# Performance work log

Hardware: AMD Instinct MI355X
Metric: run time of the kernel (lower is better)

Reference implementation:

```python
import jax, jax.numpy as jnp
import numpy as np

D_MODEL = 1024
HEADS = 16
D_K = D_MODEL // HEADS
NEG_INF = -1e10


def setup_inputs() -> dict:
    key = jax.random.key(0)
    ks = jax.random.split(key, 10)
    n, s = 2, 2048
    inp = {
        "value": jax.random.normal(ks[0], (n, s, D_MODEL), dtype=jnp.float32),
        "key": jax.random.normal(ks[1], (n, s, D_MODEL), dtype=jnp.float32),
        "query": jax.random.normal(ks[2], (n, s, D_MODEL), dtype=jnp.float32),
        "mask": jax.random.randint(ks[3], (n, 1, s, s), 0, 2, dtype=jnp.int32),
        # torch.nn.Linear weights are [out, in]; y = x @ W.T (+ b)
        "Wq": jax.random.normal(ks[4], (D_MODEL, D_MODEL), dtype=jnp.float32) * (D_MODEL ** -0.5),
        "Wk": jax.random.normal(ks[5], (D_MODEL, D_MODEL), dtype=jnp.float32) * (D_MODEL ** -0.5),
        "Wv": jax.random.normal(ks[6], (D_MODEL, D_MODEL), dtype=jnp.float32) * (D_MODEL ** -0.5),
        "Wo": jax.random.normal(ks[7], (D_MODEL, D_MODEL), dtype=jnp.float32) * (D_MODEL ** -0.5),
        "bo": jax.random.normal(ks[8], (D_MODEL,), dtype=jnp.float32) * 0.01,
    }
    return inp


def reference(value, key, query, mask, Wq, Wk, Wv, Wo, bo):
    n, q_len, _ = query.shape
    # projections (Linear, no bias): x @ W.T
    q = (query @ Wq.T).reshape(n, q_len, HEADS, D_K)
    k = (key @ Wk.T).reshape(n, key.shape[1], HEADS, D_K)
    v = (value @ Wv.T).reshape(n, value.shape[1], HEADS, D_K)
    scores = jnp.einsum('nqhd,nkhd->nhqk', q, k)  # [n,h,q,k]
    scores = jnp.where(mask == 0, jnp.float32(NEG_INF), scores)
    attn = jax.nn.softmax(scores / jnp.sqrt(jnp.float32(D_K)), axis=-1)
    out = jnp.einsum('nhql,nlhd->nqhd', attn, v).reshape(n, q_len, D_MODEL)
    return out @ Wo.T + bo
```

## Files before the change

kernel.cpp:

```cpp
#include <hip/hip_runtime.h>
#include <hip/hip_bf16.h>
#include <stdint.h>

#define SEQ     2048
#define NBATCH  2
#define DMODEL  1024
#define NH      16
#define DKH     64

typedef __bf16 bf16;
typedef __attribute__((ext_vector_type(8))) __bf16 bf16x8;
typedef __attribute__((ext_vector_type(4))) __bf16 bf16x4;
typedef __attribute__((ext_vector_type(4))) float  f32x4;

static __device__ __forceinline__ f32x4 mfma16(bf16x8 a, bf16x8 b, f32x4 c) {
    return __builtin_amdgcn_mfma_f32_16x16x32_bf16(a, b, c, 0, 0, 0);
}

typedef const __attribute__((address_space(1))) void* gas_cptr;
typedef __attribute__((address_space(3))) void*       las_ptr;
#define GLDS16(g, l) __builtin_amdgcn_global_load_lds((gas_cptr)(g), (las_ptr)(l), 16, 0, 0)

__global__ __launch_bounds__(256) void cvt_all_k(const float* __restrict__ q,
                                                 const float* __restrict__ k,
                                                 const float* __restrict__ v,
                                                 const float* __restrict__ wq,
                                                 const float* __restrict__ wk,
                                                 const float* __restrict__ wv,
                                                 const float* __restrict__ wo,
                                                 bf16* __restrict__ qb, bf16* __restrict__ kb,
                                                 bf16* __restrict__ vb, bf16* __restrict__ wqb,
                                                 bf16* __restrict__ wkb, bf16* __restrict__ wvb,
                                                 bf16* __restrict__ wob) {
    const float* src; bf16* dst; int n4;
    const int NX4 = (NBATCH * SEQ * DMODEL) / 4, NW4 = (DMODEL * DMODEL) / 4;
    switch (blockIdx.y) {
        case 0: src = q;  dst = qb;  n4 = NX4; break;
        case 1: src = k;  dst = kb;  n4 = NX4; break;
        case 2: src = v;  dst = vb;  n4 = NX4; break;
        case 3: src = wq; dst = wqb; n4 = NW4; break;
        case 4: src = wk; dst = wkb; n4 = NW4; break;
        case 5: src = wv; dst = wvb; n4 = NW4; break;
        default: src = wo; dst = wob; n4 = NW4; break;
    }
    int stride = gridDim.x * blockDim.x;
    for (int i = blockIdx.x * blockDim.x + threadIdx.x; i < n4; i += stride) {
        f32x4 f = ((const f32x4*)src)[i];
        bf16x4 o;
#pragma unroll
        for (int j = 0; j < 4; j++) o[j] = (bf16)f[j];
        ((bf16x4*)dst)[i] = o;
    }
}

__global__ __launch_bounds__(256) void pack_mask_k(const int* __restrict__ mask,
                                                   unsigned long long* __restrict__ bits,
                                                   int nwords) {
    int wave  = (blockIdx.x * blockDim.x + threadIdx.x) >> 6;
    int lane  = threadIdx.x & 63;
    int nwtot = (gridDim.x * blockDim.x) >> 6;
    for (int w = wave; w < nwords; w += nwtot) {
        int m = mask[(size_t)w * 64 + lane];
        unsigned long long b = __ballot(m != 0);
        if (lane == 0) bits[w] = b;
    }
}

__global__ __launch_bounds__(256) void qkv_gemm(const bf16* __restrict__ Xq,
                                                const bf16* __restrict__ Xk,
                                                const bf16* __restrict__ Xv,
                                                const bf16* __restrict__ Wq,
                                                const bf16* __restrict__ Wk,
                                                const bf16* __restrict__ Wv,
                                                bf16* __restrict__ Qo,
                                                bf16* __restrict__ Ko,
                                                bf16* __restrict__ Vto) {
    __shared__ bf16 As[128 * 32], Bs[128 * 32];
    const int z = blockIdx.z;
    const bf16* A = (z == 0) ? Xq : (z == 1) ? Xk : Xv;
    const bf16* W = (z == 0) ? Wq : (z == 1) ? Wk : Wv;
    const int bm = blockIdx.x * 128, bn = blockIdx.y * 128;
    const int tid = threadIdx.x, wave = tid >> 6, lane = tid & 63;
    const int wm = wave >> 1, wn = wave & 1, lo = lane & 15, hi = lane >> 4;

    const int r0 = wave * 32 + (lane >> 2);
    const int c8 = (lane & 3) * 8;
    const bf16* Ag = A + (size_t)(bm + r0) * DMODEL + c8;
    const bf16* Bg = W + (size_t)(bn + r0) * DMODEL + c8;
    bf16* lA = &As[wave * 1024];
    bf16* lB = &Bs[wave * 1024];

    f32x4 acc[4][4];
#pragma unroll
    for (int i = 0; i < 4; i++)
#pragma unroll
        for (int j = 0; j < 4; j++) acc[i][j] = 0.0f;

    for (int k0 = 0; k0 < DMODEL; k0 += 32) {
        __syncthreads();
        GLDS16(Ag + k0, lA);
        GLDS16(Ag + k0 + (size_t)16 * DMODEL, lA + 512);
        GLDS16(Bg + k0, lB);
        GLDS16(Bg + k0 + (size_t)16 * DMODEL, lB + 512);
        __syncthreads();

        bf16x8 a[4], b[4];
#pragma unroll
        for (int t = 0; t < 4; t++) {
            a[t] = *(const bf16x8*)&As[(wm * 64 + t * 16 + lo) * 32 + hi * 8];
            b[t] = *(const bf16x8*)&Bs[(wn * 64 + t * 16 + lo) * 32 + hi * 8];
        }
#pragma unroll
        for (int tm = 0; tm < 4; tm++)
#pragma unroll
            for (int tn = 0; tn < 4; tn++)
                acc[tm][tn] = mfma16(a[tm], b[tn], acc[tm][tn]);
    }

    if (z < 2) {
        bf16* O = (z == 0) ? Qo : Ko;
#pragma unroll
        for (int tm = 0; tm < 4; tm++)
#pragma unroll
            for (int tn = 0; tn < 4; tn++)
#pragma unroll
                for (int r = 0; r < 4; r++) {
                    int m = bm + wm * 64 + tm * 16 + hi * 4 + r;
                    int o = bn + wn * 64 + tn * 16 + lo;
                    int nidx = m >> 11, sq = m & 2047;
                    int hh = o >> 6, d = o & 63;
                    O[(((size_t)nidx * NH + hh) * SEQ + sq) * DKH + d] = (bf16)acc[tm][tn][r];
                }
    } else {
#pragma unroll
        for (int tm = 0; tm < 4; tm++)
#pragma unroll
            for (int tn = 0; tn < 4; tn++)
#pragma unroll
                for (int r = 0; r < 4; r++) {
                    int m = bm + wm * 64 + tm * 16 + hi * 4 + r;
                    int o = bn + wn * 64 + tn * 16 + lo;
                    int nidx = m >> 11, sq = m & 2047;
                    int hh = o >> 6, d = o & 63;
                    Vto[(((size_t)nidx * NH + hh) * DKH + d) * SEQ + sq] = (bf16)acc[tm][tn][r];
                }
    }
}

__global__ __launch_bounds__(256, 5) void attn_k(const bf16* __restrict__ Q,
                                                 const bf16* __restrict__ K,
                                                 const bf16* __restrict__ Vt,
                                                 const unsigned long long* __restrict__ mbits,
                                                 bf16* __restrict__ Op0,
                                                 bf16* __restrict__ Op1,
                                                 float* __restrict__ Lp) {
    __shared__ bf16 Ks[64 * 72];
    __shared__ bf16 Vs[64 * 72];
    __shared__ bf16 Ps[64 * 72];

    const int bid = blockIdx.x;
    const int xcd = bid & 7, j = bid >> 3;
    const int hd = xcd * 4 + (j & 3);
    const int qb = (j >> 2) & 31;
    const int ks = j >> 7;
    const int n = hd >> 4, h = hd & 15;

    const int tid = threadIdx.x, wave = tid >> 6, lane = tid & 63;
    const int lo = lane & 15, hi = lane >> 4;

    const size_t headoff = (size_t)hd * SEQ * DKH;
    const bf16* Qh = Q + headoff;
    const bf16* Kh = K + headoff;
    const bf16* Vh = Vt + headoff;

    const int qrow = qb * 64 + wave * 16 + lo;
    const bf16x8 aq0 = *(const bf16x8*)(Qh + (size_t)qrow * DKH + hi * 8);
    const bf16x8 aq1 = *(const bf16x8*)(Qh + (size_t)qrow * DKH + 32 + hi * 8);

    bf16x8 ones;
#pragma unroll
    for (int i = 0; i < 8; i++) ones[i] = (bf16)1.0f;

    f32x4 oacc[4];
#pragma unroll
    for (int t = 0; t < 4; t++) oacc[t] = 0.0f;
    f32x4 lacc; lacc = 0.0f;

    const unsigned long long* mb = mbits + ((size_t)n * SEQ + qb * 64 + wave * 16) * (SEQ / 64);
    const float c = 0.18033688f;

    const int kbeg = ks * 1024, kend = kbeg + 1024;

    const int srow = tid >> 3, sseg = tid & 7;
    const bf16* Kg = Kh + (size_t)srow * DKH + sseg * 8;
    const bf16* Vg = Vh + (size_t)srow * SEQ + sseg * 8;

    bf16x8 rk0 = *(const bf16x8*)(Kg + (size_t)kbeg * DKH);
    bf16x8 rk1 = *(const bf16x8*)(Kg + (size_t)(kbeg + 32) * DKH);
    bf16x8 rv0 = *(const bf16x8*)(Vg + kbeg);
    bf16x8 rv1 = *(const bf16x8*)(Vg + (size_t)32 * SEQ + kbeg);

    for (int k0 = kbeg; k0 < kend; k0 += 64) {
        __syncthreads();
        *(bf16x8*)&Ks[srow * 72 + sseg * 8]        = rk0;
        *(bf16x8*)&Ks[(srow + 32) * 72 + sseg * 8] = rk1;
        *(bf16x8*)&Vs[srow * 72 + sseg * 8]        = rv0;
        *(bf16x8*)&Vs[(srow + 32) * 72 + sseg * 8] = rv1;
        if (k0 + 64 < kend) {
            rk0 = *(const bf16x8*)(Kg + (size_t)(k0 + 64) * DKH);
            rk1 = *(const bf16x8*)(Kg + (size_t)(k0 + 96) * DKH);
            rv0 = *(const bf16x8*)(Vg + k0 + 64);
            rv1 = *(const bf16x8*)(Vg + (size_t)32 * SEQ + k0 + 64);
        }
        __syncthreads();

        unsigned long long w64[4];
#pragma unroll
        for (int r = 0; r < 4; r++) w64[r] = mb[(size_t)(hi * 4 + r) * (SEQ / 64) + (k0 >> 6)];

        f32x4 s[4];
#pragma unroll
        for (int tn = 0; tn < 4; tn++) {
            const int kr = (tn * 16 + lo) * 72;
            bf16x8 b0 = *(const bf16x8*)&Ks[kr + hi * 8];
            bf16x8 b1 = *(const bf16x8*)&Ks[kr + 32 + hi * 8];
            f32x4 z4; z4 = 0.0f;
            z4 = mfma16(aq0, b0, z4);
            z4 = mfma16(aq1, b1, z4);
            s[tn] = z4;
        }

#pragma unroll
        for (int r = 0; r < 4; r++) {
            unsigned wlo = (unsigned)(w64[r] >> lo);
            unsigned whi = (unsigned)(w64[r] >> (lo + 32));
#pragma unroll
            for (int tn = 0; tn < 4; tn++) {
                unsigned bit = ((tn < 2 ? wlo : whi) >> ((tn & 1) * 16)) & 1u;
                float pv = exp2f(s[tn][r] * c);
                pv = bit ? pv : 0.0f;
                Ps[(wave * 16 + hi * 4 + r) * 72 + tn * 16 + lo] = (bf16)pv;
            }
        }
        asm volatile("s_waitcnt lgkmcnt(0)" ::: "memory");

        bf16x8 ap0 = *(const bf16x8*)&Ps[(wave * 16 + lo) * 72 + hi * 8];
        bf16x8 ap1 = *(const bf16x8*)&Ps[(wave * 16 + lo) * 72 + 32 + hi * 8];
#pragma unroll
        for (int td = 0; td < 4; td++) {
            bf16x8 b0 = *(const bf16x8*)&Vs[(td * 16 + lo) * 72 + hi * 8];
            bf16x8 b1 = *(const bf16x8*)&Vs[(td * 16 + lo) * 72 + 32 + hi * 8];
            oacc[td] = mfma16(ap0, b0, oacc[td]);
            oacc[td] = mfma16(ap1, b1, oacc[td]);
        }
        lacc = mfma16(ap0, ones, lacc);
        lacc = mfma16(ap1, ones, lacc);
    }

    bf16* Op = ks ? Op1 : Op0;
#pragma unroll
    for (int td = 0; td < 4; td++)
#pragma unroll
        for (int r = 0; r < 4; r++) {
            int q = qb * 64 + wave * 16 + hi * 4 + r;
            int d = td * 16 + lo;
            Op[((size_t)n * SEQ + q) * DMODEL + h * 64 + d] = (bf16)oacc[td][r];
        }
    if (lo == 0) {
#pragma unroll
        for (int r = 0; r < 4; r++) {
            int q = qb * 64 + wave * 16 + hi * 4 + r;
            Lp[(size_t)ks * (NBATCH * NH * SEQ) + ((size_t)(n * NH + h) * SEQ) + q] = lacc[r];
        }
    }
}

__global__ __launch_bounds__(256) void merge_k(const bf16* __restrict__ o0,
                                               const bf16* __restrict__ o1,
                                               const float* __restrict__ lp,
                                               bf16* __restrict__ Aout) {
    int t = blockIdx.x * blockDim.x + threadIdx.x;
    int q = t >> 7;
    int h = (t >> 3) & 15;
    int n = q >> 11;
    bf16x8 a = ((const bf16x8*)o0)[t];
    bf16x8 b = ((const bf16x8*)o1)[t];
    int li = (n * NH + h) * SEQ + (q & 2047);
    float l = lp[li] + lp[NBATCH * NH * SEQ + li];
    float rl = 1.0f / l;
    bf16x8 o;
#pragma unroll
    for (int i = 0; i < 8; i++) o[i] = (bf16)(((float)a[i] + (float)b[i]) * rl);
    ((bf16x8*)Aout)[t] = o;
}

__global__ __launch_bounds__(256) void out_gemm(const bf16* __restrict__ A,
                                                const bf16* __restrict__ W,
                                                const float* __restrict__ bias,
                                                float* __restrict__ Out) {
    __shared__ bf16 As[128 * 32], Bs[128 * 32];
    const int bm = blockIdx.x * 128, bn = blockIdx.y * 128;
    const int tid = threadIdx.x, wave = tid >> 6, lane = tid & 63;
    const int wm = wave >> 1, wn = wave & 1, lo = lane & 15, hi = lane >> 4;

    const int r0 = wave * 32 + (lane >> 2);
    const int c8 = (lane & 3) * 8;
    const bf16* Ag = A + (size_t)(bm + r0) * DMODEL + c8;
    const bf16* Bg = W + (size_t)(bn + r0) * DMODEL + c8;
    bf16* lA = &As[wave * 1024];
    bf16* lB = &Bs[wave * 1024];

    f32x4 acc[4][4];
#pragma unroll
    for (int i = 0; i < 4; i++)
#pragma unroll
        for (int j = 0; j < 4; j++) acc[i][j] = 0.0f;

    for (int k0 = 0; k0 < DMODEL; k0 += 32) {
        __syncthreads();
        GLDS16(Ag + k0, lA);
        GLDS16(Ag + k0 + (size_t)16 * DMODEL, lA + 512);
        GLDS16(Bg + k0, lB);
        GLDS16(Bg + k0 + (size_t)16 * DMODEL, lB + 512);
        __syncthreads();

        bf16x8 a[4], b[4];
#pragma unroll
        for (int t = 0; t < 4; t++) {
            a[t] = *(const bf16x8*)&As[(wm * 64 + t * 16 + lo) * 32 + hi * 8];
            b[t] = *(const bf16x8*)&Bs[(wn * 64 + t * 16 + lo) * 32 + hi * 8];
        }
#pragma unroll
        for (int tm = 0; tm < 4; tm++)
#pragma unroll
            for (int tn = 0; tn < 4; tn++)
                acc[tm][tn] = mfma16(a[tm], b[tn], acc[tm][tn]);
    }

#pragma unroll
    for (int tm = 0; tm < 4; tm++)
#pragma unroll
        for (int tn = 0; tn < 4; tn++) {
            int o = bn + wn * 64 + tn * 16 + lo;
            float bv = bias[o];
#pragma unroll
            for (int r = 0; r < 4; r++) {
                int m = bm + wm * 64 + tm * 16 + hi * 4 + r;
                Out[(size_t)m * DMODEL + o] = acc[tm][tn][r] + bv;
            }
        }
}

extern "C" void kernel_launch(void* const* d_in, const int* in_sizes, int n_in,
                              void* d_out, int out_size, void* d_ws, size_t ws_size,
                              hipStream_t stream) {
    const float* value = (const float*)d_in[0];
    const float* key   = (const float*)d_in[1];
    const float* query = (const float*)d_in[2];
    const int*   mask  = (const int*)d_in[3];
    const float* Wq    = (const float*)d_in[4];
    const float* Wk    = (const float*)d_in[5];
    const float* Wv    = (const float*)d_in[6];
    const float* Wo    = (const float*)d_in[7];
    const float* bo    = (const float*)d_in[8];
    float* out = (float*)d_out;

    char* ws = (char*)d_ws;
    bf16* Qws = (bf16*)(ws);
    bf16* Kws = (bf16*)(ws + (8u  << 20));
    bf16* Vt  = (bf16*)(ws + (16u << 20));
    bf16* Xqb = (bf16*)(ws + (24u << 20));
    bf16* Xkb = (bf16*)(ws + (32u << 20));
    bf16* Xvb = (bf16*)(ws + (40u << 20));
    bf16* Wqb = (bf16*)(ws + (48u << 20));
    bf16* Wkb = (bf16*)(ws + (50u << 20));
    bf16* Wvb = (bf16*)(ws + (52u << 20));
    bf16* Wob = (bf16*)(ws + (54u << 20));
    unsigned long long* mbits = (unsigned long long*)(ws + (56u << 20));
    bf16*  Op0 = Xqb;
    bf16*  Op1 = Xkb;
    bf16*  Aws = Xvb;
    float* Lp  = (float*)Wqb;

    cvt_all_k<<<dim3(1024, 7), 256, 0, stream>>>(query, key, value, Wq, Wk, Wv, Wo,
                                                 Xqb, Xkb, Xvb, Wqb, Wkb, Wvb, Wob);
    pack_mask_k<<<1024, 256, 0, stream>>>(mask, mbits, NBATCH * SEQ * (SEQ / 64));
    qkv_gemm<<<dim3(32, 8, 3), 256, 0, stream>>>(Xqb, Xkb, Xvb, Wqb, Wkb, Wvb, Qws, Kws, Vt);
    attn_k<<<2048, 256, 0, stream>>>(Qws, Kws, Vt, mbits, Op0, Op1, Lp);
    merge_k<<<2048, 256, 0, stream>>>(Op0, Op1, Lp, Aws);
    out_gemm<<<dim3(32, 8), 256, 0, stream>>>(Aws, Wob, bo, out);
}
```

Before: 299.7 us.

## Fuse mask packing, deepen QKV K-step, fold softmax scale, widen attention blocks

Mask bit-packing is folded into the conversion kernel as an extra grid row, which removes one launch. The QKV GEMM now loads 64-wide K slabs per barrier pair instead of 32, halving the number of synchronisations. The softmax scale is folded into Q at projection time, so the exp in attention no longer needs a multiply. The attention kernel uses 512-thread blocks covering 128 query rows, so each K/V tile staged in shared memory is reused by twice as many waves, with one load per thread instead of two. The trade-offs are higher register and LDS pressure per block and slightly different rounding, since the scale is applied before the bf16 cast of Q.

Measured after the change: 360.1 us. 20.1% more time.

```diff
diff --git a/kernel.cpp b/kernel.cpp
--- a/kernel.cpp
+++ b/kernel.cpp
@@ -8,6 +8,8 @@
 #define NH      16
 #define DKH     64
 
+#define CSCALE  0.18033688f
+
 typedef __bf16 bf16;
 typedef __attribute__((ext_vector_type(8))) __bf16 bf16x8;
 typedef __attribute__((ext_vector_type(4))) __bf16 bf16x4;
@@ -21,17 +23,31 @@
 typedef __attribute__((address_space(3))) void*       las_ptr;
 #define GLDS16(g, l) __builtin_amdgcn_global_load_lds((gas_cptr)(g), (las_ptr)(l), 16, 0, 0)
 
-__global__ __launch_bounds__(256) void cvt_all_k(const float* __restrict__ q,
-                                                 const float* __restrict__ k,
-                                                 const float* __restrict__ v,
-                                                 const float* __restrict__ wq,
-                                                 const float* __restrict__ wk,
-                                                 const float* __restrict__ wv,
-                                                 const float* __restrict__ wo,
-                                                 bf16* __restrict__ qb, bf16* __restrict__ kb,
-                                                 bf16* __restrict__ vb, bf16* __restrict__ wqb,
-                                                 bf16* __restrict__ wkb, bf16* __restrict__ wvb,
-                                                 bf16* __restrict__ wob) {
+__global__ __launch_bounds__(256) void cvt_pack_k(const float* __restrict__ q,
+                                                  const float* __restrict__ k,
+                                                  const float* __restrict__ v,
+                                                  const float* __restrict__ wq,
+                                                  const float* __restrict__ wk,
+                                                  const float* __restrict__ wv,
+                                                  const float* __restrict__ wo,
+                                                  const int* __restrict__ mask,
+                                                  bf16* __restrict__ qb, bf16* __restrict__ kb,
+                                                  bf16* __restrict__ vb, bf16* __restrict__ wqb,
+                                                  bf16* __restrict__ wkb, bf16* __restrict__ wvb,
+                                                  bf16* __restrict__ wob,
+                                                  unsigned long long* __restrict__ bits) {
+    if (blockIdx.y == 7) {
+        const int nwords = NBATCH * SEQ * (SEQ / 64);
+        int wave  = (blockIdx.x * blockDim.x + threadIdx.x) >> 6;
+        int lane  = threadIdx.x & 63;
+        int nwtot = (gridDim.x * blockDim.x) >> 6;
+        for (int w = wave; w < nwords; w += nwtot) {
+            int m = mask[(size_t)w * 64 + lane];
+            unsigned long long b = __ballot(m != 0);
+            if (lane == 0) bits[w] = b;
+        }
+        return;
+    }
     const float* src; bf16* dst; int n4;
     const int NX4 = (NBATCH * SEQ * DMODEL) / 4, NW4 = (DMODEL * DMODEL) / 4;
     switch (blockIdx.y) {
@@ -53,19 +69,6 @@
     }
 }
 
-__global__ __launch_bounds__(256) void pack_mask_k(const int* __restrict__ mask,
-                                                   unsigned long long* __restrict__ bits,
-                                                   int nwords) {
-    int wave  = (blockIdx.x * blockDim.x + threadIdx.x) >> 6;
-    int lane  = threadIdx.x & 63;
-    int nwtot = (gridDim.x * blockDim.x) >> 6;
-    for (int w = wave; w < nwords; w += nwtot) {
-        int m = mask[(size_t)w * 64 + lane];
-        unsigned long long b = __ballot(m != 0);
-        if (lane == 0) bits[w] = b;
-    }
-}
-
 __global__ __launch_bounds__(256) void qkv_gemm(const bf16* __restrict__ Xq,
                                                 const bf16* __restrict__ Xk,
                                                 const bf16* __restrict__ Xv,
@@ -75,7 +78,7 @@
                                                 bf16* __restrict__ Qo,
                                                 bf16* __restrict__ Ko,
                                                 bf16* __restrict__ Vto) {
-    __shared__ bf16 As[128 * 32], Bs[128 * 32];
+    __shared__ bf16 As0[128 * 32], As1[128 * 32], Bs0[128 * 32], Bs1[128 * 32];
     const int z = blockIdx.z;
     const bf16* A = (z == 0) ? Xq : (z == 1) ? Xk : Xv;
     const bf16* W = (z == 0) ? Wq : (z == 1) ? Wk : Wv;
@@ -87,8 +90,7 @@
     const int c8 = (lane & 3) * 8;
     const bf16* Ag = A + (size_t)(bm + r0) * DMODEL + c8;
     const bf16* Bg = W + (size_t)(bn + r0) * DMODEL + c8;
-    bf16* lA = &As[wave * 1024];
-    bf16* lB = &Bs[wave * 1024];
+    const int lof = wave * 1024;
 
     f32x4 acc[4][4];
 #pragma unroll
@@ -96,27 +98,42 @@
 #pragma unroll
         for (int j = 0; j < 4; j++) acc[i][j] = 0.0f;
 
-    for (int k0 = 0; k0 < DMODEL; k0 += 32) {
-        __syncthreads();
-        GLDS16(Ag + k0, lA);
-        GLDS16(Ag + k0 + (size_t)16 * DMODEL, lA + 512);
-        GLDS16(Bg + k0, lB);
-        GLDS16(Bg + k0 + (size_t)16 * DMODEL, lB + 512);
+    for (int k0 = 0; k0 < DMODEL; k0 += 64) {
+        __syncthreads();
+        GLDS16(Ag + k0,                          As0 + lof);
+        GLDS16(Ag + k0 + (size_t)16 * DMODEL,    As0 + lof + 512);
+        GLDS16(Ag + k0 + 32,                     As1 + lof);
+        GLDS16(Ag + k0 + 32 + (size_t)16 * DMODEL, As1 + lof + 512);
+        GLDS16(Bg + k0,                          Bs0 + lof);
+        GLDS16(Bg + k0 + (size_t)16 * DMODEL,    Bs0 + lof + 512);
+        GLDS16(Bg + k0 + 32,                     Bs1 + lof);
+        GLDS16(Bg + k0 + 32 + (size_t)16 * DMODEL, Bs1 + lof + 512);
         __syncthreads();
 
         bf16x8 a[4], b[4];
 #pragma unroll
         for (int t = 0; t < 4; t++) {
-            a[t] = *(const bf16x8*)&As[(wm * 64 + t * 16 + lo) * 32 + hi * 8];
-            b[t] = *(const bf16x8*)&Bs[(wn * 64 + t * 16 + lo) * 32 + hi * 8];
+            a[t] = *(const bf16x8*)&As0[(wm * 64 + t * 16 + lo) * 32 + hi * 8];
+            b[t] = *(const bf16x8*)&Bs0[(wn * 64 + t * 16 + lo) * 32 + hi * 8];
         }
 #pragma unroll
         for (int tm = 0; tm < 4; tm++)
 #pragma unroll
             for (int tn = 0; tn < 4; tn++)
                 acc[tm][tn] = mfma16(a[tm], b[tn], acc[tm][tn]);
-    }
-
+#pragma unroll
+        for (int t = 0; t < 4; t++) {
+            a[t] = *(const bf16x8*)&As1[(wm * 64 + t * 16 + lo) * 32 + hi * 8];
+            b[t] = *(const bf16x8*)&Bs1[(wn * 64 + t * 16 + lo) * 32 + hi * 8];
+        }
+#pragma unroll
+        for (int tm = 0; tm < 4; tm++)
+#pragma unroll
+            for (int tn = 0; tn < 4; tn++)
+                acc[tm][tn] = mfma16(a[tm], b[tn], acc[tm][tn]);
+    }
+
+    const float osc = (z == 0) ? CSCALE : 1.0f;
     if (z < 2) {
         bf16* O = (z == 0) ? Qo : Ko;
 #pragma unroll
@@ -129,7 +146,7 @@
                     int o = bn + wn * 64 + tn * 16 + lo;
                     int nidx = m >> 11, sq = m & 2047;
                     int hh = o >> 6, d = o & 63;
-                    O[(((size_t)nidx * NH + hh) * SEQ + sq) * DKH + d] = (bf16)acc[tm][tn][r];
+                    O[(((size_t)nidx * NH + hh) * SEQ + sq) * DKH + d] = (bf16)(acc[tm][tn][r] * osc);
                 }
     } else {
 #pragma unroll
@@ -147,7 +164,7 @@
     }
 }
 
-__global__ __launch_bounds__(256, 5) void attn_k(const bf16* __restrict__ Q,
+__global__ __launch_bounds__(512, 8) void attn_k(const bf16* __restrict__ Q,
                                                  const bf16* __restrict__ K,
                                                  const bf16* __restrict__ Vt,
                                                  const unsigned long long* __restrict__ mbits,
@@ -156,13 +173,13 @@
                                                  float* __restrict__ Lp) {
     __shared__ bf16 Ks[64 * 72];
     __shared__ bf16 Vs[64 * 72];
-    __shared__ bf16 Ps[64 * 72];
+    __shared__ bf16 Ps[128 * 72];
 
     const int bid = blockIdx.x;
     const int xcd = bid & 7, j = bid >> 3;
     const int hd = xcd * 4 + (j & 3);
-    const int qb = (j >> 2) & 31;
-    const int ks = j >> 7;
+    const int qb = (j >> 2) & 15;
+    const int ks = j >> 6;
     const int n = hd >> 4, h = hd & 15;
 
     const int tid = threadIdx.x, wave = tid >> 6, lane = tid & 63;
@@ -173,7 +190,7 @@
     const bf16* Kh = K + headoff;
     const bf16* Vh = Vt + headoff;
 
-    const int qrow = qb * 64 + wave * 16 + lo;
+    const int qrow = qb * 128 + wave * 16 + lo;
     const bf16x8 aq0 = *(const bf16x8*)(Qh + (size_t)qrow * DKH + hi * 8);
     const bf16x8 aq1 = *(const bf16x8*)(Qh + (size_t)qrow * DKH + 32 + hi * 8);
 
@@ -186,31 +203,25 @@
     for (int t = 0; t < 4; t++) oacc[t] = 0.0f;
     f32x4 lacc; lacc = 0.0f;
 
-    const unsigned long long* mb = mbits + ((size_t)n * SEQ + qb * 64 + wave * 16) * (SEQ / 64);
-    const float c = 0.18033688f;
+    const unsigned long long* mb = mbits + ((size_t)n * SEQ + qb * 128 + wave * 16) * (SEQ / 64);
 
     const int kbeg = ks * 1024, kend = kbeg + 1024;
 
     const int srow = tid >> 3, sseg = tid & 7;
     const bf16* Kg = Kh + (size_t)srow * DKH + sseg * 8;
     const bf16* Vg = Vh + (size_t)srow * SEQ + sseg * 8;
-
-    bf16x8 rk0 = *(const bf16x8*)(Kg + (size_t)kbeg * DKH);
-    bf16x8 rk1 = *(const bf16x8*)(Kg + (size_t)(kbeg + 32) * DKH);
-    bf16x8 rv0 = *(const bf16x8*)(Vg + kbeg);
-    bf16x8 rv1 = *(const bf16x8*)(Vg + (size_t)32 * SEQ + kbeg);
+    const int si = srow * 72 + sseg * 8;
+
+    bf16x8 rk = *(const bf16x8*)(Kg + (size_t)kbeg * DKH);
+    bf16x8 rv = *(const bf16x8*)(Vg + kbeg);
 
     for (int k0 = kbeg; k0 < kend; k0 += 64) {
         __syncthreads();
-        *(bf16x8*)&Ks[srow * 72 + sseg * 8]        = rk0;
-        *(bf16x8*)&Ks[(srow + 32) * 72 + sseg * 8] = rk1;
-        *(bf16x8*)&Vs[srow * 72 + sseg * 8]        = rv0;
-        *(bf16x8*)&Vs[(srow + 32) * 72 + sseg * 8] = rv1;
+        *(bf16x8*)&Ks[si] = rk;
+        *(bf16x8*)&Vs[si] = rv;
         if (k0 + 64 < kend) {
-            rk0 = *(const bf16x8*)(Kg + (size_t)(k0 + 64) * DKH);
-            rk1 = *(const bf16x8*)(Kg + (size_t)(k0 + 96) * DKH);
-            rv0 = *(const bf16x8*)(Vg + k0 + 64);
-            rv1 = *(const bf16x8*)(Vg + (size_t)32 * SEQ + k0 + 64);
+            rk = *(const bf16x8*)(Kg + (size_t)(k0 + 64) * DKH);
+            rv = *(const bf16x8*)(Vg + k0 + 64);
         }
         __syncthreads();
 
@@ -237,7 +248,7 @@
 #pragma unroll
             for (int tn = 0; tn < 4; tn++) {
                 unsigned bit = ((tn < 2 ? wlo : whi) >> ((tn & 1) * 16)) & 1u;
-                float pv = exp2f(s[tn][r] * c);
+                float pv = exp2f(s[tn][r]);
                 pv = bit ? pv : 0.0f;
                 Ps[(wave * 16 + hi * 4 + r) * 72 + tn * 16 + lo] = (bf16)pv;
             }
@@ -262,14 +273,14 @@
     for (int td = 0; td < 4; td++)
 #pragma unroll
         for (int r = 0; r < 4; r++) {
-            int q = qb * 64 + wave * 16 + hi * 4 + r;
+            int q = qb * 128 + wave * 16 + hi * 4 + r;
             int d = td * 16 + lo;
             Op[((size_t)n * SEQ + q) * DMODEL + h * 64 + d] = (bf16)oacc[td][r];
         }
     if (lo == 0) {
 #pragma unroll
         for (int r = 0; r < 4; r++) {
-            int q = qb * 64 + wave * 16 + hi * 4 + r;
+            int q = qb * 128 + wave * 16 + hi * 4 + r;
             Lp[(size_t)ks * (NBATCH * NH * SEQ) + ((size_t)(n * NH + h) * SEQ) + q] = lacc[r];
         }
     }
@@ -382,11 +393,10 @@
     bf16*  Aws = Xvb;
     float* Lp  = (float*)Wqb;
 
-    cvt_all_k<<<dim3(1024, 7), 256, 0, stream>>>(query, key, value, Wq, Wk, Wv, Wo,
-                                                 Xqb, Xkb, Xvb, Wqb, Wkb, Wvb, Wob);
-    pack_mask_k<<<1024, 256, 0, stream>>>(mask, mbits, NBATCH * SEQ * (SEQ / 64));
+    cvt_pack_k<<<dim3(1024, 8), 256, 0, stream>>>(query, key, value, Wq, Wk, Wv, Wo, mask,
+                                                  Xqb, Xkb, Xvb, Wqb, Wkb, Wvb, Wob, mbits);
     qkv_gemm<<<dim3(32, 8, 3), 256, 0, stream>>>(Xqb, Xkb, Xvb, Wqb, Wkb, Wvb, Qws, Kws, Vt);
-    attn_k<<<2048, 256, 0, stream>>>(Qws, Kws, Vt, mbits, Op0, Op1, Lp);
+    attn_k<<<1024, 512, 0, stream>>>(Qws, Kws, Vt, mbits, Op0, Op1, Lp);
     merge_k<<<2048, 256, 0, stream>>>(Op0, Op1, Lp, Aws);
     out_gemm<<<dim3(32, 8), 256, 0, stream>>>(Aws, Wob, bo, out);
 }
```
